# Kernel tuning notes

Measured on AMD Instinct MI355X. Metric: run time of the kernel, lower is better.

The kernel has to match this reference:

```python
import jax, jax.numpy as jnp
import numpy as np

N, E = 50000, 400000
IN, H, EF = 128, 64, 16


def _lin(k, fan_in, fan_out):
    # kaiming_normal_(fan_in, leaky_relu) approx gain
    return jax.random.normal(k, (fan_in, fan_out), jnp.float32) * (2.0 / fan_in) ** 0.5


def setup_inputs():
    key = jax.random.key(0)
    ks = jax.random.split(key, 24)
    inp = {
        "x": jax.random.normal(ks[0], (N, IN), jnp.float32),
        "edge_index": jax.random.randint(ks[1], (2, E), 0, N, dtype=jnp.int32),
        "edge_attr": jax.random.normal(ks[2], (E, EF), jnp.float32),
        # GCNConv layers (weight + bias)
        "W1": _lin(ks[3], IN, H),        "b1": jnp.zeros((H,), jnp.float32),
        "W2": _lin(ks[4], H, 2 * H),     "b2": jnp.zeros((2 * H,), jnp.float32),
        "W3": _lin(ks[5], 2 * H, 4 * H), "b3": jnp.zeros((4 * H,), jnp.float32),
        # edge encoder
        "We": _lin(ks[6], EF, H),        "be": jnp.zeros((H,), jnp.float32),
        # edge_features MLP: (4H*2 + H) -> 2H -> H
        "Wf1": _lin(ks[7], 4 * H * 2 + H, 2 * H), "bf1": jnp.zeros((2 * H,), jnp.float32),
        "Wf2": _lin(ks[8], 2 * H, H),             "bf2": jnp.zeros((H,), jnp.float32),
        # trade classifier: H -> H -> 1 (sigmoid)
        "Wc1": _lin(ks[9], H, H),  "bc1": jnp.zeros((H,), jnp.float32),
        "Wc2": _lin(ks[10], H, 1), "bc2": jnp.zeros((1,), jnp.float32),
        "Wr1": _lin(ks[11], H, H),  "br1": jnp.zeros((H,), jnp.float32),
        "Wr2": _lin(ks[12], H, 1), "br2": jnp.zeros((1,), jnp.float32),
    }
    return inp


def _lrelu(v):
    return jax.nn.leaky_relu(v, 0.01)


def _gcn_conv(x, src, dst, W, b):
    """PyG GCNConv: add self-loops, D^-1/2 (A+I) D^-1/2 X W + b."""
    n = x.shape[0]
    sl = jnp.arange(n, dtype=src.dtype)
    s = jnp.concatenate([src, sl])
    d = jnp.concatenate([dst, sl])
    deg = jax.ops.segment_sum(jnp.ones(s.shape[0], x.dtype), d, num_segments=n)
    dinv = jnp.where(deg > 0, jax.lax.rsqrt(deg), 0.0)
    norm = dinv[s] * dinv[d]                    # [E+N]
    xw = x @ W                                  # [N, out]
    out = jax.ops.segment_sum(xw[s] * norm[:, None], d, num_segments=n)
    return out + b


def reference(x, edge_index, edge_attr, W1, b1, W2, b2, W3, b3, We, be,
              Wf1, bf1, Wf2, bf2, Wc1, bc1, Wc2, bc2, Wr1, br1, Wr2, br2):
    src, dst = edge_index[0], edge_index[1]
    edge_enc = _lrelu(edge_attr @ We + be)                  # [E, H]
    h1 = _lrelu(_gcn_conv(x, src, dst, W1, b1))             # [N, H]
    h2 = _lrelu(_gcn_conv(h1, src, dst, W2, b2))            # [N, 2H]
    h3 = _lrelu(_gcn_conv(h2, src, dst, W3, b3))            # [N, 4H]
    combined = jnp.concatenate([h3[src], h3[dst], edge_enc], axis=1)  # [E, 9H]
    common = _lrelu(combined @ Wf1 + bf1) @ Wf2 + bf2       # [E, H]
    trade_exists = jax.nn.sigmoid(_lrelu(common @ Wc1 + bc1) @ Wc2 + bc2)  # [E, 1]
    trade_value = _lrelu(common @ Wr1 + br1) @ Wr2 + br2    # [E, 1]
    final_pred = trade_exists * trade_value
    return (final_pred, trade_exists)
```

## Files before the change

### kernel.cpp

```cpp
#include <hip/hip_runtime.h>
#include <math.h>

#define N_NODES 50000
#define N_EDGES 400000

__device__ __forceinline__ float lrelu(float v) { return v > 0.0f ? v : 0.01f * v; }

__global__ __launch_bounds__(256) void k_degi(const int* __restrict__ dstv,
                                              int* __restrict__ degi) {
  int e = blockIdx.x * 256 + threadIdx.x;
  if (e < N_EDGES) atomicAdd(&degi[dstv[e]], 1);
}

__global__ __launch_bounds__(1024) void k_scan(const int* __restrict__ degi,
                                               int* __restrict__ rowptr,
                                               float* __restrict__ dinv) {
  __shared__ int swsum[16], swoff[16];
  const int t = threadIdx.x;
  const int lane = t & 63, w = t >> 6;
  int run = 0;
  for (int base = 0; base < N_NODES; base += 1024) {
    int i = base + t;
    int v = (i < N_NODES) ? degi[i] : 0;
    int x = v;
#pragma unroll
    for (int off = 1; off < 64; off <<= 1) {
      int y = __shfl_up(x, off, 64);
      if (lane >= off) x += y;
    }
    if (lane == 63) swsum[w] = x;
    __syncthreads();
    if (t < 16) {
      int s = swsum[t];
      int si = s;
#pragma unroll
      for (int off = 1; off < 16; off <<= 1) {
        int y = __shfl_up(si, off, 16);
        if (t >= off) si += y;
      }
      swoff[t] = si - s;
      if (t == 15) swsum[15] = si;
    }
    __syncthreads();
    if (i < N_NODES) {
      rowptr[i] = run + swoff[w] + x - v;
      dinv[i] = rsqrtf((float)(v + 1));
    }
    int tot = swsum[15];
    __syncthreads();
    run += tot;
  }
  if (t == 0) rowptr[N_NODES] = run;
}

__global__ __launch_bounds__(256) void k_slot(const int* __restrict__ srcv,
                                              const int* __restrict__ dstv,
                                              const int* __restrict__ rowptr,
                                              int* __restrict__ cnt,
                                              int* __restrict__ csr_src) {
  int e = blockIdx.x * 256 + threadIdx.x;
  if (e < N_EDGES) {
    int d = dstv[e];
    int pos = rowptr[d] + atomicAdd(&cnt[d], 1);
    csr_src[pos] = srcv[e];
  }
}

__global__ __launch_bounds__(256, 4) void k_gemm(const float* __restrict__ A,
                                                 const float* __restrict__ W,
                                                 const float* __restrict__ rowscale,
                                                 float* __restrict__ C,
                                                 int M, int K, int Nc) {
  __shared__ float At[32][128];
  __shared__ float Bt[32][64];
  const int rb = blockIdx.x * 128, cb = blockIdx.y * 64;
  const int t = threadIdx.x;
  const int tr = t & 15, tc = t >> 4;
  const int rA = tr * 4, rB = 64 + tr * 4, c0 = tc * 4;
  float acc[8][4] = {};
  for (int kb = 0; kb < K; kb += 32) {
    __syncthreads();
    {
      int r = t & 127, kq = t >> 7;
      int row = rb + r; if (row >= M) row = M - 1;
      const float* ap = A + (size_t)row * K + kb + kq * 16;
#pragma unroll
      for (int u = 0; u < 4; u++) {
        float4 v = *(const float4*)(ap + u * 4);
        At[kq * 16 + u * 4 + 0][r] = v.x;
        At[kq * 16 + u * 4 + 1][r] = v.y;
        At[kq * 16 + u * 4 + 2][r] = v.z;
        At[kq * 16 + u * 4 + 3][r] = v.w;
      }
    }
    {
#pragma unroll
      for (int j = 0; j < 2; j++) {
        int f = t + j * 256;
        int r = f >> 4, c4 = (f & 15) * 4;
        *(float4*)&Bt[r][c4] = *(const float4*)(W + (size_t)(kb + r) * Nc + cb + c4);
      }
    }
    __syncthreads();
#pragma unroll 8
    for (int k = 0; k < 32; k++) {
      float4 a0 = *(const float4*)&At[k][rA];
      float4 a1 = *(const float4*)&At[k][rB];
      float4 b  = *(const float4*)&Bt[k][c0];
      float av[8] = {a0.x, a0.y, a0.z, a0.w, a1.x, a1.y, a1.z, a1.w};
      float bv[4] = {b.x, b.y, b.z, b.w};
#pragma unroll
      for (int i = 0; i < 8; i++)
#pragma unroll
        for (int j = 0; j < 4; j++)
          acc[i][j] = fmaf(av[i], bv[j], acc[i][j]);
    }
  }
#pragma unroll
  for (int i = 0; i < 4; i++) {
    int r = rb + rA + i;
    if (r < M) {
      float sc = rowscale[r];
      float4 v = {acc[i][0] * sc, acc[i][1] * sc, acc[i][2] * sc, acc[i][3] * sc};
      *(float4*)(C + (size_t)r * Nc + cb + c0) = v;
    }
  }
#pragma unroll
  for (int i = 0; i < 4; i++) {
    int r = rb + rB + i;
    if (r < M) {
      float sc = rowscale[r];
      float4 v = {acc[4 + i][0] * sc, acc[4 + i][1] * sc, acc[4 + i][2] * sc, acc[4 + i][3] * sc};
      *(float4*)(C + (size_t)r * Nc + cb + c0) = v;
    }
  }
}

template <int F>
__global__ __launch_bounds__(256) void k_gather(const float* __restrict__ xs,
                                                const int* __restrict__ rowptr,
                                                const int* __restrict__ csr_src,
                                                const float* __restrict__ dinv,
                                                const float* __restrict__ b,
                                                float* __restrict__ h) {
  constexpr int NPB = 256 / F;
  const int node = blockIdx.x * NPB + threadIdx.x / F;
  const int f = threadIdx.x & (F - 1);
  if (node >= N_NODES) return;
  const int beg = rowptr[node], end = rowptr[node + 1];
  float acc = xs[(size_t)node * F + f];
  int k = beg;
  for (; k + 4 <= end; k += 4) {
    int s0 = csr_src[k], s1 = csr_src[k + 1], s2 = csr_src[k + 2], s3 = csr_src[k + 3];
    float a0 = xs[(size_t)s0 * F + f];
    float a1 = xs[(size_t)s1 * F + f];
    float a2 = xs[(size_t)s2 * F + f];
    float a3 = xs[(size_t)s3 * F + f];
    acc += a0 + a1 + a2 + a3;
  }
  for (; k < end; k++) acc += xs[(size_t)csr_src[k] * F + f];
  h[(size_t)node * F + f] = lrelu(acc * dinv[node] + b[f]);
}

struct FusedSMem {
  int src[64], dst[64];
  float We[16 * 64];
  float be[64];
  union {
    struct { float A[32][64]; float B[32][128]; } p1;
    float T1t[128][68];
  } u;
};

__global__ __launch_bounds__(256, 4) void k_fused(
    const float* __restrict__ h3, const int* __restrict__ srcv, const int* __restrict__ dstv,
    const float* __restrict__ eattr, const float* __restrict__ Weg, const float* __restrict__ beg_,
    const float* __restrict__ Wf1, const float* __restrict__ bf1,
    const float* __restrict__ Wf2g, const float* __restrict__ bf2,
    float* __restrict__ common) {
  __shared__ FusedSMem sm;
  const int t = threadIdx.x;
  const int eb = blockIdx.x * 64;

  if (t < 64) sm.src[t] = srcv[eb + t];
  else if (t < 128) sm.dst[t - 64] = dstv[eb + t - 64];
  else if (t < 192) sm.be[t - 128] = beg_[t - 128];
  *(float4*)&sm.We[t * 4] = *(const float4*)(Weg + t * 4);
  __syncthreads();

  const int te = t & 15, tc = t >> 4;
  const int e0 = te * 4;
  const int cA = tc * 4, cB = 64 + tc * 4;
  float acc[4][8] = {};

  for (int ck = 0; ck < 18; ck++) {
    __syncthreads();
    const int kb = ck * 32;
    const int e = t & 63, kq = t >> 6;
    if (ck < 16) {
      int row = (ck < 8) ? sm.src[e] : sm.dst[e];
      int colb = (ck < 8) ? kb : kb - 256;
      const float* p = h3 + (size_t)row * 256 + colb + kq * 8;
      float4 v0 = *(const float4*)p;
      float4 v1 = *(const float4*)(p + 4);
      float* ac = &sm.u.p1.A[kq * 8][0];
      ac[0 * 64 + e] = v0.x; ac[1 * 64 + e] = v0.y; ac[2 * 64 + e] = v0.z; ac[3 * 64 + e] = v0.w;
      ac[4 * 64 + e] = v1.x; ac[5 * 64 + e] = v1.y; ac[6 * 64 + e] = v1.z; ac[7 * 64 + e] = v1.w;
    } else {
      float eav[16];
      const float* ep = eattr + (size_t)(eb + e) * 16;
#pragma unroll
      for (int u = 0; u < 4; u++) {
        float4 v = *(const float4*)(ep + u * 4);
        eav[u * 4 + 0] = v.x; eav[u * 4 + 1] = v.y; eav[u * 4 + 2] = v.z; eav[u * 4 + 3] = v.w;
      }
      int ob = (ck - 16) * 32 + kq * 8;
#pragma unroll
      for (int j = 0; j < 8; j++) {
        float val = sm.be[ob + j];
#pragma unroll
        for (int i = 0; i < 16; i++) val = fmaf(eav[i], sm.We[i * 64 + ob + j], val);
        sm.u.p1.A[kq * 8 + j][e] = lrelu(val);
      }
    }
    {
#pragma unroll
      for (int j = 0; j < 4; j++) {
        int f = t + j * 256;
        int r = f >> 5, c4 = (f & 31) * 4;
        *(float4*)&sm.u.p1.B[r][c4] = *(const float4*)(Wf1 + (size_t)(kb + r) * 128 + c4);
      }
    }
    __syncthreads();
#pragma unroll 8
    for (int k = 0; k < 32; k++) {
      float4 a4 = *(const float4*)&sm.u.p1.A[k][e0];
      float4 b0 = *(const float4*)&sm.u.p1.B[k][cA];
      float4 b1 = *(const float4*)&sm.u.p1.B[k][cB];
      float av[4] = {a4.x, a4.y, a4.z, a4.w};
      float bv[8] = {b0.x, b0.y, b0.z, b0.w, b1.x, b1.y, b1.z, b1.w};
#pragma unroll
      for (int i = 0; i < 4; i++)
#pragma unroll
        for (int j = 0; j < 8; j++)
          acc[i][j] = fmaf(av[i], bv[j], acc[i][j]);
    }
  }
  __syncthreads();
#pragma unroll
  for (int j = 0; j < 4; j++) {
    float bj = bf1[cA + j];
#pragma unroll
    for (int i = 0; i < 4; i++)
      sm.u.T1t[cA + j][e0 + i] = lrelu(acc[i][j] + bj);
  }
#pragma unroll
  for (int j = 0; j < 4; j++) {
    float bj = bf1[cB + j];
#pragma unroll
    for (int i = 0; i < 4; i++)
      sm.u.T1t[cB + j][e0 + i] = lrelu(acc[i][4 + j] + bj);
  }
  __syncthreads();
  const int e0b = (t & 15) * 4, c0b = (t >> 4) * 4;
  float a2[4][4];
#pragma unroll
  for (int j = 0; j < 4; j++) {
    float bj = bf2[c0b + j];
    a2[0][j] = bj; a2[1][j] = bj; a2[2][j] = bj; a2[3][j] = bj;
  }
#pragma unroll 8
  for (int k = 0; k < 128; k++) {
    float4 a4 = *(const float4*)&sm.u.T1t[k][e0b];
    float4 b4 = *(const float4*)(Wf2g + k * 64 + c0b);
    float av[4] = {a4.x, a4.y, a4.z, a4.w};
    float bv[4] = {b4.x, b4.y, b4.z, b4.w};
#pragma unroll
    for (int i = 0; i < 4; i++)
#pragma unroll
      for (int j = 0; j < 4; j++)
        a2[i][j] = fmaf(av[i], bv[j], a2[i][j]);
  }
#pragma unroll
  for (int i = 0; i < 4; i++) {
    float4 v = {a2[i][0], a2[i][1], a2[i][2], a2[i][3]};
    *(float4*)(common + (size_t)(eb + e0b + i) * 64 + c0b) = v;
  }
}

__global__ __launch_bounds__(256, 2) void k_heads(
    const float* __restrict__ common,
    const float* __restrict__ Wc1, const float* __restrict__ bc1,
    const float* __restrict__ Wc2, const float* __restrict__ bc2,
    const float* __restrict__ Wr1, const float* __restrict__ br1,
    const float* __restrict__ Wr2, const float* __restrict__ br2,
    float* __restrict__ out) {
  const int lane = threadIdx.x & 63;
  const int wid = blockIdx.x * 4 + (threadIdx.x >> 6);
  const int nw = gridDim.x * 4;
  float wc1r[64], wr1r[64];
#pragma unroll
  for (int k = 0; k < 64; k++) {
    wc1r[k] = Wc1[k * 64 + lane];
    wr1r[k] = Wr1[k * 64 + lane];
  }
  const float bc1r = bc1[lane], br1r = br1[lane];
  const float wc2r = Wc2[lane], wr2r = Wr2[lane];
  const float bc2s = bc2[0], br2s = br2[0];
  for (int e = wid; e < N_EDGES; e += nw) {
    float cr = common[(size_t)e * 64 + lane];
    float accC = bc1r, accR = br1r;
#pragma unroll
    for (int k = 0; k < 64; k++) {
      float cv = __shfl(cr, k, 64);
      accC = fmaf(cv, wc1r[k], accC);
      accR = fmaf(cv, wr1r[k], accR);
    }
    float pc = lrelu(accC) * wc2r;
    float pr = lrelu(accR) * wr2r;
#pragma unroll
    for (int off = 32; off > 0; off >>= 1) {
      pc += __shfl_xor(pc, off, 64);
      pr += __shfl_xor(pr, off, 64);
    }
    if (lane == 0) {
      float te = 1.0f / (1.0f + expf(-(pc + bc2s)));
      float tv = pr + br2s;
      out[e] = te * tv;
      out[N_EDGES + e] = te;
    }
  }
}

extern "C" void kernel_launch(void* const* d_in, const int* in_sizes, int n_in,
                              void* d_out, int out_size, void* d_ws, size_t ws_size,
                              hipStream_t stream) {
  const float* x     = (const float*)d_in[0];
  const int*   eidx  = (const int*)d_in[1];
  const float* eattr = (const float*)d_in[2];
  const float* W1 = (const float*)d_in[3];  const float* b1 = (const float*)d_in[4];
  const float* W2 = (const float*)d_in[5];  const float* b2 = (const float*)d_in[6];
  const float* W3 = (const float*)d_in[7];  const float* b3 = (const float*)d_in[8];
  const float* We = (const float*)d_in[9];  const float* be = (const float*)d_in[10];
  const float* Wf1 = (const float*)d_in[11]; const float* bf1 = (const float*)d_in[12];
  const float* Wf2 = (const float*)d_in[13]; const float* bf2 = (const float*)d_in[14];
  const float* Wc1 = (const float*)d_in[15]; const float* bc1 = (const float*)d_in[16];
  const float* Wc2 = (const float*)d_in[17]; const float* bc2 = (const float*)d_in[18];
  const float* Wr1 = (const float*)d_in[19]; const float* br1 = (const float*)d_in[20];
  const float* Wr2 = (const float*)d_in[21]; const float* br2 = (const float*)d_in[22];
  const int* srcv = eidx;
  const int* dstv = eidx + N_EDGES;
  float* outp = (float*)d_out;

  int* ip = (int*)d_ws;
  int* degi    = ip;
  int* rowptr  = ip + 50048;
  int* cnt     = ip + 100096;
  int* csr_src = ip + 150144;
  float* fp = (float*)d_ws + 550400;
  size_t o = 0;
  float* dinv = fp + o; o += 50048;
  float* xs1  = fp + o; o += (size_t)N_NODES * 64;
  float* h1   = fp + o; o += (size_t)N_NODES * 64;
  float* xs2  = fp + o; o += (size_t)N_NODES * 128;
  float* h2   = fp + o; o += (size_t)N_NODES * 128;
  float* xs3  = fp + o; o += (size_t)N_NODES * 256;
  float* h3   = fp + o; o += (size_t)N_NODES * 256;
  float* common = xs1;

  hipMemsetAsync(degi, 0, 50048 * sizeof(int), stream);
  hipMemsetAsync(cnt, 0, 50048 * sizeof(int), stream);
  k_degi<<<(N_EDGES + 255) / 256, 256, 0, stream>>>(dstv, degi);
  k_scan<<<1, 1024, 0, stream>>>(degi, rowptr, dinv);
  k_slot<<<(N_EDGES + 255) / 256, 256, 0, stream>>>(srcv, dstv, rowptr, cnt, csr_src);

  k_gemm<<<dim3(391, 1), 256, 0, stream>>>(x, W1, dinv, xs1, N_NODES, 128, 64);
  k_gather<64><<<N_NODES / 4, 256, 0, stream>>>(xs1, rowptr, csr_src, dinv, b1, h1);

  k_gemm<<<dim3(391, 2), 256, 0, stream>>>(h1, W2, dinv, xs2, N_NODES, 64, 128);
  k_gather<128><<<N_NODES / 2, 256, 0, stream>>>(xs2, rowptr, csr_src, dinv, b2, h2);

  k_gemm<<<dim3(391, 4), 256, 0, stream>>>(h2, W3, dinv, xs3, N_NODES, 128, 256);
  k_gather<256><<<N_NODES, 256, 0, stream>>>(xs3, rowptr, csr_src, dinv, b3, h3);

  k_fused<<<N_EDGES / 64, 256, 0, stream>>>(h3, srcv, dstv, eattr, We, be,
                                            Wf1, bf1, Wf2, bf2, common);
  k_heads<<<768, 256, 0, stream>>>(common, Wc1, bc1, Wc2, bc2, Wr1, br1, Wr2, br2, outp);
}
```

Baseline: 1.956 ms.

## Widen fused edge MLP kernel to 512 threads with padded shared tiles

The fused edge-MLP kernel goes from 256 to 512 threads per block. Each thread's register tile shrinks from 4x8 to 4x4 in the first GEMM and from 4x4 to 4x2 in the second. The gather now uses one float4 per thread over 8 segments per edge. The shared A and B tiles are padded to reduce bank conflicts. The aim is more parallelism and lower register pressure for higher occupancy, at the cost of more shared-memory traffic per FMA and smaller per-thread reuse.

```diff
diff --git a/kernel.cpp b/kernel.cpp
--- a/kernel.cpp
+++ b/kernel.cpp
@@ -167,12 +167,12 @@
   float We[16 * 64];
   float be[64];
   union {
-    struct { float A[32][64]; float B[32][128]; } p1;
+    struct { float A[32][68]; float B[32][132]; } p1;
     float T1t[128][68];
   } u;
 };
 
-__global__ __launch_bounds__(256, 4) void k_fused(
+__global__ __launch_bounds__(512, 8) void k_fused(
     const float* __restrict__ h3, const int* __restrict__ srcv, const int* __restrict__ dstv,
     const float* __restrict__ eattr, const float* __restrict__ Weg, const float* __restrict__ beg_,
     const float* __restrict__ Wf1, const float* __restrict__ bf1,
@@ -185,48 +185,46 @@
   if (t < 64) sm.src[t] = srcv[eb + t];
   else if (t < 128) sm.dst[t - 64] = dstv[eb + t - 64];
   else if (t < 192) sm.be[t - 128] = beg_[t - 128];
-  *(float4*)&sm.We[t * 4] = *(const float4*)(Weg + t * 4);
+  if (t < 256) *(float4*)&sm.We[t * 4] = *(const float4*)(Weg + t * 4);
   __syncthreads();
 
   const int te = t & 15, tc = t >> 4;
-  const int e0 = te * 4;
-  const int cA = tc * 4, cB = 64 + tc * 4;
-  float acc[4][8] = {};
+  const int e0 = te * 4, c0 = tc * 4;
+  const int el = t >> 3, seg = t & 7;
+  float acc[4][4] = {};
 
   for (int ck = 0; ck < 18; ck++) {
     __syncthreads();
     const int kb = ck * 32;
-    const int e = t & 63, kq = t >> 6;
     if (ck < 16) {
-      int row = (ck < 8) ? sm.src[e] : sm.dst[e];
+      int row = (ck < 8) ? sm.src[el] : sm.dst[el];
       int colb = (ck < 8) ? kb : kb - 256;
-      const float* p = h3 + (size_t)row * 256 + colb + kq * 8;
-      float4 v0 = *(const float4*)p;
-      float4 v1 = *(const float4*)(p + 4);
-      float* ac = &sm.u.p1.A[kq * 8][0];
-      ac[0 * 64 + e] = v0.x; ac[1 * 64 + e] = v0.y; ac[2 * 64 + e] = v0.z; ac[3 * 64 + e] = v0.w;
-      ac[4 * 64 + e] = v1.x; ac[5 * 64 + e] = v1.y; ac[6 * 64 + e] = v1.z; ac[7 * 64 + e] = v1.w;
+      float4 v = *(const float4*)(h3 + (size_t)row * 256 + colb + seg * 4);
+      sm.u.p1.A[seg * 4 + 0][el] = v.x;
+      sm.u.p1.A[seg * 4 + 1][el] = v.y;
+      sm.u.p1.A[seg * 4 + 2][el] = v.z;
+      sm.u.p1.A[seg * 4 + 3][el] = v.w;
     } else {
       float eav[16];
-      const float* ep = eattr + (size_t)(eb + e) * 16;
+      const float* ep = eattr + (size_t)(eb + el) * 16;
 #pragma unroll
       for (int u = 0; u < 4; u++) {
         float4 v = *(const float4*)(ep + u * 4);
         eav[u * 4 + 0] = v.x; eav[u * 4 + 1] = v.y; eav[u * 4 + 2] = v.z; eav[u * 4 + 3] = v.w;
       }
-      int ob = (ck - 16) * 32 + kq * 8;
-#pragma unroll
-      for (int j = 0; j < 8; j++) {
+      int ob = (ck - 16) * 32 + seg * 4;
+#pragma unroll
+      for (int j = 0; j < 4; j++) {
         float val = sm.be[ob + j];
 #pragma unroll
         for (int i = 0; i < 16; i++) val = fmaf(eav[i], sm.We[i * 64 + ob + j], val);
-        sm.u.p1.A[kq * 8 + j][e] = lrelu(val);
+        sm.u.p1.A[seg * 4 + j][el] = lrelu(val);
       }
     }
     {
 #pragma unroll
-      for (int j = 0; j < 4; j++) {
-        int f = t + j * 256;
+      for (int j = 0; j < 2; j++) {
+        int f = t + j * 512;
         int r = f >> 5, c4 = (f & 31) * 4;
         *(float4*)&sm.u.p1.B[r][c4] = *(const float4*)(Wf1 + (size_t)(kb + r) * 128 + c4);
       }
@@ -235,56 +233,47 @@
 #pragma unroll 8
     for (int k = 0; k < 32; k++) {
       float4 a4 = *(const float4*)&sm.u.p1.A[k][e0];
-      float4 b0 = *(const float4*)&sm.u.p1.B[k][cA];
-      float4 b1 = *(const float4*)&sm.u.p1.B[k][cB];
+      float4 b4 = *(const float4*)&sm.u.p1.B[k][c0];
       float av[4] = {a4.x, a4.y, a4.z, a4.w};
-      float bv[8] = {b0.x, b0.y, b0.z, b0.w, b1.x, b1.y, b1.z, b1.w};
+      float bv[4] = {b4.x, b4.y, b4.z, b4.w};
 #pragma unroll
       for (int i = 0; i < 4; i++)
 #pragma unroll
-        for (int j = 0; j < 8; j++)
+        for (int j = 0; j < 4; j++)
           acc[i][j] = fmaf(av[i], bv[j], acc[i][j]);
     }
   }
   __syncthreads();
 #pragma unroll
   for (int j = 0; j < 4; j++) {
-    float bj = bf1[cA + j];
+    float bj = bf1[c0 + j];
 #pragma unroll
     for (int i = 0; i < 4; i++)
-      sm.u.T1t[cA + j][e0 + i] = lrelu(acc[i][j] + bj);
-  }
-#pragma unroll
-  for (int j = 0; j < 4; j++) {
-    float bj = bf1[cB + j];
-#pragma unroll
-    for (int i = 0; i < 4; i++)
-      sm.u.T1t[cB + j][e0 + i] = lrelu(acc[i][4 + j] + bj);
+      sm.u.T1t[c0 + j][e0 + i] = lrelu(acc[i][j] + bj);
   }
   __syncthreads();
-  const int e0b = (t & 15) * 4, c0b = (t >> 4) * 4;
-  float a2[4][4];
-#pragma unroll
-  for (int j = 0; j < 4; j++) {
+  const int e0b = (t & 15) * 4, c0b = (t >> 4) * 2;
+  float a2[4][2];
+#pragma unroll
+  for (int j = 0; j < 2; j++) {
     float bj = bf2[c0b + j];
     a2[0][j] = bj; a2[1][j] = bj; a2[2][j] = bj; a2[3][j] = bj;
   }
 #pragma unroll 8
   for (int k = 0; k < 128; k++) {
     float4 a4 = *(const float4*)&sm.u.T1t[k][e0b];
-    float4 b4 = *(const float4*)(Wf2g + k * 64 + c0b);
+    float2 w2 = *(const float2*)(Wf2g + k * 64 + c0b);
     float av[4] = {a4.x, a4.y, a4.z, a4.w};
-    float bv[4] = {b4.x, b4.y, b4.z, b4.w};
-#pragma unroll
-    for (int i = 0; i < 4; i++)
-#pragma unroll
-      for (int j = 0; j < 4; j++)
-        a2[i][j] = fmaf(av[i], bv[j], a2[i][j]);
+#pragma unroll
+    for (int i = 0; i < 4; i++) {
+      a2[i][0] = fmaf(av[i], w2.x, a2[i][0]);
+      a2[i][1] = fmaf(av[i], w2.y, a2[i][1]);
+    }
   }
 #pragma unroll
   for (int i = 0; i < 4; i++) {
-    float4 v = {a2[i][0], a2[i][1], a2[i][2], a2[i][3]};
-    *(float4*)(common + (size_t)(eb + e0b + i) * 64 + c0b) = v;
+    float2 v = {a2[i][0], a2[i][1]};
+    *(float2*)(common + (size_t)(eb + e0b + i) * 64 + c0b) = v;
   }
 }
 
@@ -383,7 +372,7 @@
   k_gemm<<<dim3(391, 4), 256, 0, stream>>>(h2, W3, dinv, xs3, N_NODES, 128, 256);
   k_gather<256><<<N_NODES, 256, 0, stream>>>(xs3, rowptr, csr_src, dinv, b3, h3);
 
-  k_fused<<<N_EDGES / 64, 256, 0, stream>>>(h3, srcv, dstv, eattr, We, be,
+  k_fused<<<N_EDGES / 64, 512, 0, stream>>>(h3, srcv, dstv, eattr, We, be,
                                             Wf1, bf1, Wf2, bf2, common);
   k_heads<<<768, 256, 0, stream>>>(common, Wc1, bc1, Wc2, bc2, Wr1, br1, Wr2, br2, outp);
 }
```

New measurement: 2.481 ms. 1.27x slower.
